# Kernel optimization log

Measured on AMD Instinct MI355X. Metric: run time of the kernel, lower is better.

The kernel has to match this reference:

```python
import jax, jax.numpy as jnp
import numpy as np

N, E, B, H, L = 50000, 500000, 64, 64, 4


def setup_inputs() -> dict:
    key = jax.random.key(0)
    ks = jax.random.split(key, 32)
    def w(k, shp, fan_in):
        s = 1.0 / np.sqrt(fan_in)
        return jax.random.uniform(k, shp, jnp.float32, -s, s)
    inp = {
        "v0": jax.random.normal(ks[0], (N, 1), jnp.float32),
        "v1": jax.random.normal(ks[1], (N, 1), jnp.float32),
        "dist": jax.random.uniform(ks[2], (E, 1), jnp.float32),
        "edge_index": jax.random.randint(ks[3], (2, E), 0, N, jnp.int32),
        "batch": jnp.sort(jax.random.randint(ks[4], (N,), 0, B, jnp.int32)),
        "batch_size": B,
        # embeddings / per-input linears
        "wte": jax.random.normal(ks[5], (2, H), jnp.float32),
        "W_in0": w(ks[6], (H, 1), 1), "b_in0": w(ks[7], (H,), 1),
        "W_in1": w(ks[8], (H, 1), 1), "b_in1": w(ks[9], (H,), 1),
        "W_out0": w(ks[10], (1, H), H), "b_out0": w(ks[11], (1,), H),
        "W_out1": w(ks[12], (1, H), H), "b_out1": w(ks[13], (1,), H),
        "W_edge": w(ks[14], (H, 1), 1), "b_edge": w(ks[15], (H,), 1),
        # shared GraphBlock (ModuleList([block]*L) shares weights)
        "W_el": w(ks[16], (H, 2 * H), 2 * H), "b_el": w(ks[17], (H,), 2 * H),
        "W_n1": w(ks[18], (4 * H, 3 * H), 3 * H), "b_n1": w(ks[19], (4 * H,), 3 * H),
        "W_n2": w(ks[20], (H, 4 * H), 4 * H), "b_n2": w(ks[21], (H,), 4 * H),
        "W_gl": w(ks[22], (H, 2 * H), 2 * H), "b_gl": w(ks[23], (H,), 2 * H),
        # shared LSTMCell
        "W_ih": w(ks[24], (4 * H, H), H), "W_hh": w(ks[25], (4 * H, H), H),
        "b_ih": w(ks[26], (4 * H,), H), "b_hh": w(ks[27], (4 * H,), H),
    }
    return inp


def _forward(v0, v1, dist, edge_index, batch, batch_size,
             wte, W_in0, b_in0, W_in1, b_in1, W_out0, b_out0, W_out1, b_out1,
             W_edge, b_edge, W_el, b_el, W_n1, b_n1, W_n2, b_n2, W_gl, b_gl,
             W_ih, W_hh, b_ih, b_hh):
    # x = sum_i (type_embedding_i + Linear_i(v_i))  -> [N, H]
    x = (wte[0] + v0 @ W_in0.T + b_in0) + (wte[1] + v1 @ W_in1.T + b_in1)
    e = dist @ W_edge.T + b_edge                      # [E, H]
    u = jnp.zeros((batch_size, x.shape[-1]), x.dtype)  # [B, H]
    row, col = edge_index[0], edge_index[1]
    n_nodes = x.shape[0]
    cs = []
    for _ in range(L):  # shared weights across layers (faithful to [block]*L)
        # edge MLP on gathered source features, scatter-max to destination nodes
        msg = jax.nn.relu(jnp.concatenate([x[row], e], axis=-1) @ W_el.T + b_el)
        agg = jax.ops.segment_max(msg, col, num_segments=n_nodes)
        agg = jnp.where(jnp.isfinite(agg), agg, 0.0)  # empty segments -> 0
        # node MLP with residual
        h1 = jax.nn.relu(jnp.concatenate([agg, x, u[batch]], axis=-1) @ W_n1.T + b_n1)
        x = x + h1 @ W_n2.T + b_n2
        # global update: per-graph max over nodes
        x_u = jax.ops.segment_max(x, batch, num_segments=batch_size)
        x_u = jnp.where(jnp.isfinite(x_u), x_u, 0.0)
        u = u + jax.nn.relu(jnp.concatenate([x_u, u], axis=-1) @ W_gl.T + b_gl)
        # LSTMCell with zero initial (h, c) every layer (hidden_states=None path)
        gates = u @ W_ih.T + b_ih + b_hh  # h_prev = 0 so W_hh term vanishes
        i_g, f_g, g_g, o_g = jnp.split(gates, 4, axis=-1)
        c = jax.nn.sigmoid(i_g) * jnp.tanh(g_g)        # c_prev = 0
        u = jax.nn.sigmoid(o_g) * jnp.tanh(c)
        cs.append(c)
    outs = jnp.stack([x @ W_out0.T + b_out0, x @ W_out1.T + b_out1])  # [2, N, 1]
    return outs, jnp.stack(cs)  # ([2,N,1], [L,B,H])


def reference(v0, v1, dist, edge_index, batch, batch_size,
              wte, W_in0, b_in0, W_in1, b_in1, W_out0, b_out0, W_out1, b_out1,
              W_edge, b_edge, W_el, b_el, W_n1, b_n1, W_n2, b_n2, W_gl, b_gl,
              W_ih, W_hh, b_ih, b_hh):
    return _forward(v0, v1, dist, edge_index, batch, batch_size,
                    wte, W_in0, b_in0, W_in1, b_in1, W_out0, b_out0, W_out1, b_out1,
                    W_edge, b_edge, W_el, b_el, W_n1, b_n1, W_n2, b_n2, W_gl, b_gl,
                    W_ih, W_hh, b_ih, b_hh)
```

## Files before the change

kernel.cpp:

```cpp
#include <hip/hip_runtime.h>


typedef __attribute__((ext_vector_type(8))) short short8;
typedef __attribute__((ext_vector_type(4))) float f32x4;

__device__ __forceinline__ unsigned short f2bf(float f) {
  union { float f; unsigned u; } v; v.f = f;
  unsigned r = v.u + 0x7FFFu + ((v.u >> 16) & 1u);
  return (unsigned short)(r >> 16);
}
__device__ __forceinline__ float bf2f(unsigned short s) {
  return __uint_as_float((unsigned)s << 16);
}
__device__ __forceinline__ unsigned enc_ordered(float f) {
  unsigned u = __float_as_uint(f);
  return (u >> 31) ? ~u : (u | 0x80000000u);
}

__global__ void k_prep_pq(const float* __restrict__ W_el, const float* __restrict__ b_el,
                          const float* __restrict__ W_edge, const float* __restrict__ b_edge,
                          const float* __restrict__ wte,
                          const float* __restrict__ Wi0, const float* __restrict__ bi0,
                          const float* __restrict__ Wi1, const float* __restrict__ bi1,
                          float* __restrict__ p, float* __restrict__ q,
                          float* __restrict__ c0, float* __restrict__ c1,
                          float* __restrict__ c2) {
  int h = threadIdx.x;
  float pp = 0.f, qq = 0.f, s0 = 0.f, s1 = 0.f, s2 = 0.f;
  for (int k = 0; k < 64; ++k) {
    float w2 = W_el[h * 128 + 64 + k];
    pp += w2 * W_edge[k];
    qq += w2 * b_edge[k];
    float w1 = W_el[h * 128 + k];
    float base = wte[k] + wte[64 + k] + bi0[k] + bi1[k];
    s0 += w1 * base;
    s1 += w1 * Wi0[k];
    s2 += w1 * Wi1[k];
  }
  p[h] = pp; q[h] = qq + b_el[h];
  c0[h] = s0; c1[h] = s1; c2[h] = s2;
}

__global__ void k_init(const float* __restrict__ v0, const float* __restrict__ v1,
                       const float* __restrict__ wte,
                       const float* __restrict__ Wi0, const float* __restrict__ bi0,
                       const float* __restrict__ Wi1, const float* __restrict__ bi1,
                       const int* __restrict__ batch,
                       int* __restrict__ gstart, int* __restrict__ gend,
                       float* __restrict__ x,
                       float* __restrict__ u, unsigned* __restrict__ xu_enc,
                       unsigned short* __restrict__ W1b, unsigned short* __restrict__ W2b,
                       unsigned short* __restrict__ Welb,
                       const float* __restrict__ W_n1, const float* __restrict__ W_n2,
                       const float* __restrict__ W_el,
                       int* __restrict__ deg, int* __restrict__ cur, int N) {
  int gt = blockIdx.x * 256 + threadIdx.x;
  int NH = N * 64;
  if (gt < NH) {
    int n = gt >> 6, h = gt & 63;
    x[gt] = wte[h] + wte[64 + h] + bi0[h] + bi1[h] + v0[n] * Wi0[h] + v1[n] * Wi1[h];
    if (h == 0) {
      int bg = batch[n];
      if (n == 0 || batch[n - 1] != bg) gstart[bg] = n;
      if (n == N - 1 || batch[n + 1] != bg) gend[bg] = n + 1;
    }
    return;
  }
  int i = gt - NH;
  if (i < 4096) {
    u[i] = 0.f;
  } else if (i < 8192) {
    xu_enc[i - 4096] = 0x007FFFFFu;
  } else if (i < 8192 + 49152) {
    int j = i - 8192;
    W1b[j] = f2bf(W_n1[j]);
  } else if (i < 8192 + 49152 + 16384) {
    int j = i - 57344;
    W2b[j] = f2bf(W_n2[j]);
  } else if (i < 77824) {
    int j = i - 73728;
    Welb[j] = f2bf(W_el[(j >> 6) * 128 + (j & 63)]);
  } else if (i < 77824 + N) {
    deg[i - 77824] = 0;
  } else if (i < 77824 + 2 * N) {
    cur[i - 77824 - N] = 0;
  }
}

__global__ __launch_bounds__(256) void k_hist(const int* __restrict__ eidx,
                                              int* __restrict__ deg, int E) {
  int e = blockIdx.x * 256 + threadIdx.x;
  if (e < E) atomicAdd(&deg[eidx[E + e]], 1);
}

__global__ __launch_bounds__(256) void k_scan1(const int* __restrict__ deg,
                                               int* __restrict__ off,
                                               int* __restrict__ bsum, int N) {
  __shared__ int s[256];
  int b = blockIdx.x, t = threadIdx.x;
  int i0 = b * 512 + t * 2;
  int v0 = (i0 < N) ? deg[i0] : 0;
  int v1 = (i0 + 1 < N) ? deg[i0 + 1] : 0;
  int sum = v0 + v1;
  s[t] = sum;
  __syncthreads();
  for (int d = 1; d < 256; d <<= 1) {
    int val = (t >= d) ? s[t - d] : 0;
    __syncthreads();
    s[t] += val;
    __syncthreads();
  }
  int excl = s[t] - sum;
  if (i0 < N) off[i0] = excl + v0;
  if (i0 + 1 < N) off[i0 + 1] = excl + v0 + v1;
  if (t == 255) bsum[b] = s[t];
}

__global__ void k_scan2(int* __restrict__ bsum, int nb) {
  __shared__ int s[128];
  int t = threadIdx.x;
  int v = (t < nb) ? bsum[t] : 0;
  s[t] = v;
  __syncthreads();
  for (int d = 1; d < 128; d <<= 1) {
    int val = (t >= d) ? s[t - d] : 0;
    __syncthreads();
    s[t] += val;
    __syncthreads();
  }
  if (t < nb) bsum[t] = s[t] - v;
}

__global__ __launch_bounds__(256) void k_scatter(const int* __restrict__ eidx,
                                                 const float* __restrict__ dist,
                                                 const int* __restrict__ off,
                                                 const int* __restrict__ bsum,
                                                 int* __restrict__ cur,
                                                 uint2* __restrict__ spack, int E) {
  int e = blockIdx.x * 256 + threadIdx.x;
  if (e >= E) return;
  int c = eidx[E + e];
  int base = (c == 0) ? 0 : (off[c - 1] + bsum[(c - 1) >> 9]);
  int pos = base + atomicAdd(&cur[c], 1);
  spack[pos] = make_uint2((unsigned)eidx[e] | ((unsigned)(c & 31) << 27),
                          __float_as_uint(dist[e]));
}

#define PROC(cc, gg)                                                     \
  do {                                                                   \
    int _c = (int)(cc);                                                  \
    if (_c != ccur) {                                                    \
      if (ccur >= 0) atomicMax(&aggi[ccur * 64 + lane], __float_as_int(m)); \
      ccur = _c; m = (gg);                                               \
    } else m = fmaxf(m, (gg));                                           \
  } while (0)

template <int MODE>
__global__ __launch_bounds__(256) void k_node(
    const int* __restrict__ off, const int* __restrict__ bsum,
    const uint2* __restrict__ spack,
    const float* __restrict__ p, const float* __restrict__ q,
    const float* __restrict__ c0, const float* __restrict__ c1,
    const float* __restrict__ c2,
    const float* __restrict__ v0, const float* __restrict__ v1,
    float* __restrict__ x, unsigned short* __restrict__ y_bf,
    const int* __restrict__ batch, const float* __restrict__ u,
    const unsigned short* __restrict__ W1b, const unsigned short* __restrict__ W2b,
    const unsigned short* __restrict__ Welb,
    const float* __restrict__ b_n1, const float* __restrict__ b_n2,
    unsigned* __restrict__ xu_enc,
    float* __restrict__ bmaxA, float* __restrict__ bmaxB,
    int* __restrict__ bgidA, int* __restrict__ bgidB,
    const float* __restrict__ Wo0, const float* __restrict__ bo0,
    const float* __restrict__ Wo1, const float* __restrict__ bo1,
    float* __restrict__ outp, int N) {
  __shared__ __align__(16) char inb[32 * 384];
  __shared__ __align__(16) char h1T[32 * 512];
  __shared__ uint2 smeta[2][128];
  __shared__ int sgb[32];
  int t = threadIdx.x;
  int n0 = blockIdx.x * 32;
  int lane = t & 63, wv = t >> 6;
  int lr = lane & 15;
  int lk8 = (lane >> 4) << 3;
  int jo = (lane >> 4) << 2;
  int swzr = (lr & 7) << 4;
  int h0 = wv * 16 + jo;

  float4 xo[2];
#pragma unroll
  for (int nt = 0; nt < 2; ++nt) {
    int node = n0 + nt * 16 + lr;
    xo[nt] = (node < N) ? *(const float4*)(x + (size_t)node * 64 + h0)
                        : make_float4(0.f, 0.f, 0.f, 0.f);
  }
  int nd_s = t >> 3, ko = t & 7;
  int node_s = n0 + nd_s;
  float4 ua = make_float4(0.f, 0.f, 0.f, 0.f), ub = ua;
  if (node_s < N) {
    int g = batch[node_s];
    const float4* u4 = (const float4*)u;
    ua = u4[g * 16 + ko * 2];
    ub = u4[g * 16 + ko * 2 + 1];
  }
  if (t < 32) sgb[t] = batch[min(n0 + t, N - 1)];
  float pv = p[lane], qv = q[lane];
  float c0v = 0.f, c1v = 0.f, c2v = 0.f;
  if (MODE == 0) { c0v = c0[lane]; c1v = c1[lane]; c2v = c2[lane]; }

  int* aggi = (int*)h1T;
#pragma unroll
  for (int i = 0; i < 8; ++i) aggi[t + i * 256] = 0;

#pragma unroll
  for (int nt = 0; nt < 2; ++nt) {
    int nd = nt * 16 + lr;
    unsigned lo = (unsigned)f2bf(xo[nt].x) | ((unsigned)f2bf(xo[nt].y) << 16);
    unsigned hi = (unsigned)f2bf(xo[nt].z) | ((unsigned)f2bf(xo[nt].w) << 16);
    *(uint2*)(inb + nd * 384 + ((128 + h0 * 2) ^ ((nd & 7) << 4))) = make_uint2(lo, hi);
  }
  {
    int swz = (nd_s & 7) << 4;
    uint4 uv;
    uv.x = f2bf(ua.x) | ((unsigned)f2bf(ua.y) << 16);
    uv.y = f2bf(ua.z) | ((unsigned)f2bf(ua.w) << 16);
    uv.z = f2bf(ub.x) | ((unsigned)f2bf(ub.y) << 16);
    uv.w = f2bf(ub.z) | ((unsigned)f2bf(ub.w) << 16);
    *(uint4*)(inb + nd_s * 384 + ((256 + ko * 16) ^ swz)) = uv;
  }

  {
    int last = min(n0 + 31, N - 1);
    int ebase = (n0 == 0) ? 0 : (off[n0 - 1] + bsum[(n0 - 1) >> 9]);
    int eend = off[last] + bsum[last >> 9];
    int total = eend - ebase;
    int nch = (total + 127) >> 7;
    if (t < 128 && t < total) smeta[0][t] = spack[ebase + t];
    float m = 0.f;
    int ccur = -1;
    __syncthreads();
    for (int c = 0; c < nch; ++c) {
      int cb = c << 7;
      int cnt = min(128, total - cb);
      if (c + 1 < nch) {
        int rem = total - cb - 128;
        if (t < 128 && t < rem) smeta[(c + 1) & 1][t] = spack[ebase + cb + 128 + t];
      }
      const uint2* sm = smeta[c & 1];
      int i = wv * 32;
      int i1 = min(i + 32, cnt);
      for (; i + 8 <= i1; i += 8) {
        uint2 e0 = sm[i], e1 = sm[i + 1], e2 = sm[i + 2], e3 = sm[i + 3];
        uint2 e4 = sm[i + 4], e5 = sm[i + 5], e6 = sm[i + 6], e7 = sm[i + 7];
        float y0, y1, y2, y3, y4, y5, y6, y7;
        if (MODE == 0) {
          int r0 = e0.x & 0x07FFFFFFu, r1 = e1.x & 0x07FFFFFFu;
          int r2 = e2.x & 0x07FFFFFFu, r3 = e3.x & 0x07FFFFFFu;
          int r4 = e4.x & 0x07FFFFFFu, r5 = e5.x & 0x07FFFFFFu;
          int r6 = e6.x & 0x07FFFFFFu, r7 = e7.x & 0x07FFFFFFu;
          y0 = fmaf(v1[r0], c2v, fmaf(v0[r0], c1v, c0v));
          y1 = fmaf(v1[r1], c2v, fmaf(v0[r1], c1v, c0v));
          y2 = fmaf(v1[r2], c2v, fmaf(v0[r2], c1v, c0v));
          y3 = fmaf(v1[r3], c2v, fmaf(v0[r3], c1v, c0v));
          y4 = fmaf(v1[r4], c2v, fmaf(v0[r4], c1v, c0v));
          y5 = fmaf(v1[r5], c2v, fmaf(v0[r5], c1v, c0v));
          y6 = fmaf(v1[r6], c2v, fmaf(v0[r6], c1v, c0v));
          y7 = fmaf(v1[r7], c2v, fmaf(v0[r7], c1v, c0v));
        } else {
          y0 = bf2f(y_bf[(int)((e0.x & 0x07FFFFFFu) << 6) + lane]);
          y1 = bf2f(y_bf[(int)((e1.x & 0x07FFFFFFu) << 6) + lane]);
          y2 = bf2f(y_bf[(int)((e2.x & 0x07FFFFFFu) << 6) + lane]);
          y3 = bf2f(y_bf[(int)((e3.x & 0x07FFFFFFu) << 6) + lane]);
          y4 = bf2f(y_bf[(int)((e4.x & 0x07FFFFFFu) << 6) + lane]);
          y5 = bf2f(y_bf[(int)((e5.x & 0x07FFFFFFu) << 6) + lane]);
          y6 = bf2f(y_bf[(int)((e6.x & 0x07FFFFFFu) << 6) + lane]);
          y7 = bf2f(y_bf[(int)((e7.x & 0x07FFFFFFu) << 6) + lane]);
        }
        float g0 = fmaxf(fmaf(__uint_as_float(e0.y), pv, y0 + qv), 0.f);
        float g1 = fmaxf(fmaf(__uint_as_float(e1.y), pv, y1 + qv), 0.f);
        float g2 = fmaxf(fmaf(__uint_as_float(e2.y), pv, y2 + qv), 0.f);
        float g3 = fmaxf(fmaf(__uint_as_float(e3.y), pv, y3 + qv), 0.f);
        float g4 = fmaxf(fmaf(__uint_as_float(e4.y), pv, y4 + qv), 0.f);
        float g5 = fmaxf(fmaf(__uint_as_float(e5.y), pv, y5 + qv), 0.f);
        float g6 = fmaxf(fmaf(__uint_as_float(e6.y), pv, y6 + qv), 0.f);
        float g7 = fmaxf(fmaf(__uint_as_float(e7.y), pv, y7 + qv), 0.f);
        PROC(e0.x >> 27, g0); PROC(e1.x >> 27, g1);
        PROC(e2.x >> 27, g2); PROC(e3.x >> 27, g3);
        PROC(e4.x >> 27, g4); PROC(e5.x >> 27, g5);
        PROC(e6.x >> 27, g6); PROC(e7.x >> 27, g7);
      }
      for (; i < i1; ++i) {
        uint2 e0 = sm[i];
        float y0;
        if (MODE == 0) {
          int r0 = e0.x & 0x07FFFFFFu;
          y0 = fmaf(v1[r0], c2v, fmaf(v0[r0], c1v, c0v));
        } else {
          y0 = bf2f(y_bf[(int)((e0.x & 0x07FFFFFFu) << 6) + lane]);
        }
        float g0 = fmaxf(fmaf(__uint_as_float(e0.y), pv, y0 + qv), 0.f);
        PROC(e0.x >> 27, g0);
      }
      __syncthreads();
    }
    if (ccur >= 0) atomicMax(&aggi[ccur * 64 + lane], __float_as_int(m));
  }
  __syncthreads();

  {
    int swz = (nd_s & 7) << 4;
    const float4* ag4 = (const float4*)(h1T);
    float4 aa = ag4[nd_s * 16 + ko * 2];
    float4 ab = ag4[nd_s * 16 + ko * 2 + 1];
    uint4 av;
    av.x = f2bf(aa.x) | ((unsigned)f2bf(aa.y) << 16);
    av.y = f2bf(aa.z) | ((unsigned)f2bf(aa.w) << 16);
    av.z = f2bf(ab.x) | ((unsigned)f2bf(ab.y) << 16);
    av.w = f2bf(ab.z) | ((unsigned)f2bf(ab.w) << 16);
    *(uint4*)(inb + nd_s * 384 + ((ko * 16) ^ swz)) = av;
  }
  __syncthreads();

  int w = wv;

  f32x4 acc[4][2];
#pragma unroll
  for (int ot = 0; ot < 4; ++ot)
#pragma unroll
    for (int nt = 0; nt < 2; ++nt) acc[ot][nt] = (f32x4){0.f, 0.f, 0.f, 0.f};
  const unsigned short* W1p = W1b + (w * 64 + lr) * 192 + lk8;
#pragma unroll
  for (int ks = 0; ks < 6; ++ks) {
    int kb = ks * 64 + lk8 * 2;
    short8 b0 = *(const short8*)(inb + lr * 384 + (kb ^ swzr));
    short8 b1 = *(const short8*)(inb + (16 + lr) * 384 + (kb ^ swzr));
#pragma unroll
    for (int ot = 0; ot < 4; ++ot) {
      short8 a = *(const short8*)(W1p + ot * (16 * 192) + ks * 32);
      acc[ot][0] = __builtin_amdgcn_mfma_f32_16x16x32_bf16(a, b0, acc[ot][0], 0, 0, 0);
      acc[ot][1] = __builtin_amdgcn_mfma_f32_16x16x32_bf16(a, b1, acc[ot][1], 0, 0, 0);
    }
  }
  __syncthreads();
#pragma unroll
  for (int ot = 0; ot < 4; ++ot) {
    int o = w * 64 + ot * 16 + jo;
    float4 bs = *(const float4*)(b_n1 + o);
#pragma unroll
    for (int nt = 0; nt < 2; ++nt) {
      int nd = nt * 16 + lr;
      unsigned lo = (unsigned)f2bf(fmaxf(acc[ot][nt][0] + bs.x, 0.f)) |
                    ((unsigned)f2bf(fmaxf(acc[ot][nt][1] + bs.y, 0.f)) << 16);
      unsigned hi = (unsigned)f2bf(fmaxf(acc[ot][nt][2] + bs.z, 0.f)) |
                    ((unsigned)f2bf(fmaxf(acc[ot][nt][3] + bs.w, 0.f)) << 16);
      *(uint2*)(h1T + nd * 512 + ((o * 2) ^ ((nd & 7) << 4))) = make_uint2(lo, hi);
    }
  }
  __syncthreads();

  f32x4 acc2[2] = {{0.f, 0.f, 0.f, 0.f}, {0.f, 0.f, 0.f, 0.f}};
  const unsigned short* W2p = W2b + (w * 16 + lr) * 256 + lk8;
#pragma unroll
  for (int ks = 0; ks < 8; ++ks) {
    short8 a = *(const short8*)(W2p + ks * 32);
    int kb = ks * 64 + lk8 * 2;
    short8 b0 = *(const short8*)(h1T + lr * 512 + (kb ^ swzr));
    short8 b1 = *(const short8*)(h1T + (16 + lr) * 512 + (kb ^ swzr));
    acc2[0] = __builtin_amdgcn_mfma_f32_16x16x32_bf16(a, b0, acc2[0], 0, 0, 0);
    acc2[1] = __builtin_amdgcn_mfma_f32_16x16x32_bf16(a, b1, acc2[1], 0, 0, 0);
  }
  float4 b2 = *(const float4*)(b_n2 + h0);
  char* xnb = inb;
  float4 xn[2];
#pragma unroll
  for (int nt = 0; nt < 2; ++nt) {
    int nd = nt * 16 + lr;
    int node = n0 + nd;
    xn[nt].x = xo[nt].x + acc2[nt][0] + b2.x;
    xn[nt].y = xo[nt].y + acc2[nt][1] + b2.y;
    xn[nt].z = xo[nt].z + acc2[nt][2] + b2.z;
    xn[nt].w = xo[nt].w + acc2[nt][3] + b2.w;
    if (node >= N) xn[nt] = make_float4(0.f, 0.f, 0.f, 0.f);
    if (MODE != 2 && node < N) *(float4*)(x + (size_t)node * 64 + h0) = xn[nt];
    if (MODE != 2) {
      unsigned lo = (unsigned)f2bf(xn[nt].x) | ((unsigned)f2bf(xn[nt].y) << 16);
      unsigned hi = (unsigned)f2bf(xn[nt].z) | ((unsigned)f2bf(xn[nt].w) << 16);
      *(uint2*)(xnb + nd * 128 + ((h0 * 2) ^ ((nd & 7) << 4))) = make_uint2(lo, hi);
    }
  }

  {
    const float NEG = -__builtin_huge_valf();
    int gA = sgb[0], gB = sgb[31];
    float a0 = NEG, a1 = NEG, a2 = NEG, a3 = NEG;
    float e0 = NEG, e1 = NEG, e2 = NEG, e3 = NEG;
#pragma unroll
    for (int nt = 0; nt < 2; ++nt) {
      int nd = nt * 16 + lr;
      if (n0 + nd < N) {
        int g = sgb[nd];
        if (g == gA) {
          a0 = fmaxf(a0, xn[nt].x); a1 = fmaxf(a1, xn[nt].y);
          a2 = fmaxf(a2, xn[nt].z); a3 = fmaxf(a3, xn[nt].w);
        } else if (g == gB) {
          e0 = fmaxf(e0, xn[nt].x); e1 = fmaxf(e1, xn[nt].y);
          e2 = fmaxf(e2, xn[nt].z); e3 = fmaxf(e3, xn[nt].w);
        } else {
          unsigned* xe = xu_enc + g * 64 + h0;
          atomicMax(xe + 0, enc_ordered(xn[nt].x));
          atomicMax(xe + 1, enc_ordered(xn[nt].y));
          atomicMax(xe + 2, enc_ordered(xn[nt].z));
          atomicMax(xe + 3, enc_ordered(xn[nt].w));
        }
      }
    }
#pragma unroll
    for (int msk = 1; msk <= 8; msk <<= 1) {
      a0 = fmaxf(a0, __shfl_xor(a0, msk)); a1 = fmaxf(a1, __shfl_xor(a1, msk));
      a2 = fmaxf(a2, __shfl_xor(a2, msk)); a3 = fmaxf(a3, __shfl_xor(a3, msk));
      e0 = fmaxf(e0, __shfl_xor(e0, msk)); e1 = fmaxf(e1, __shfl_xor(e1, msk));
      e2 = fmaxf(e2, __shfl_xor(e2, msk)); e3 = fmaxf(e3, __shfl_xor(e3, msk));
    }
    if (lr == 0) {
      size_t base = (size_t)blockIdx.x * 64 + h0;
      bmaxA[base + 0] = a0; bmaxA[base + 1] = a1;
      bmaxA[base + 2] = a2; bmaxA[base + 3] = a3;
      bmaxB[base + 0] = e0; bmaxB[base + 1] = e1;
      bmaxB[base + 2] = e2; bmaxB[base + 3] = e3;
    }
    if (t == 0) {
      bgidA[blockIdx.x] = gA;
      bgidB[blockIdx.x] = (gB == gA) ? -1 : gB;
    }
  }
  __syncthreads();

  if (MODE != 2) {
    f32x4 acc3[2] = {{0.f, 0.f, 0.f, 0.f}, {0.f, 0.f, 0.f, 0.f}};
    const unsigned short* W3p = Welb + (w * 16 + lr) * 64 + lk8;
#pragma unroll
    for (int ks = 0; ks < 2; ++ks) {
      short8 a = *(const short8*)(W3p + ks * 32);
      int kb = ks * 64 + lk8 * 2;
      short8 b0 = *(const short8*)(xnb + lr * 128 + (kb ^ swzr));
      short8 b1 = *(const short8*)(xnb + (16 + lr) * 128 + (kb ^ swzr));
      acc3[0] = __builtin_amdgcn_mfma_f32_16x16x32_bf16(a, b0, acc3[0], 0, 0, 0);
      acc3[1] = __builtin_amdgcn_mfma_f32_16x16x32_bf16(a, b1, acc3[1], 0, 0, 0);
    }
    int o0 = w * 16 + jo;
#pragma unroll
    for (int nt = 0; nt < 2; ++nt) {
      int node = n0 + nt * 16 + lr;
      if (node < N) {
        unsigned lo = (unsigned)f2bf(acc3[nt][0]) | ((unsigned)f2bf(acc3[nt][1]) << 16);
        unsigned hi = (unsigned)f2bf(acc3[nt][2]) | ((unsigned)f2bf(acc3[nt][3]) << 16);
        *(uint2*)(y_bf + (size_t)node * 64 + o0) = make_uint2(lo, hi);
      }
    }
  } else {
    float4 w0 = *(const float4*)(Wo0 + h0);
    float4 w1 = *(const float4*)(Wo1 + h0);
    float* ow = (float*)h1T;
#pragma unroll
    for (int nt = 0; nt < 2; ++nt) {
      float p0 = xn[nt].x * w0.x + xn[nt].y * w0.y + xn[nt].z * w0.z + xn[nt].w * w0.w;
      float p1 = xn[nt].x * w1.x + xn[nt].y * w1.y + xn[nt].z * w1.z + xn[nt].w * w1.w;
      p0 += __shfl_xor(p0, 16); p0 += __shfl_xor(p0, 32);
      p1 += __shfl_xor(p1, 16); p1 += __shfl_xor(p1, 32);
      if (lane < 16) {
        ow[w * 64 + 0 + nt * 16 + lr] = p0;
        ow[w * 64 + 32 + nt * 16 + lr] = p1;
      }
    }
    __syncthreads();
    if (t < 64) {
      int oi = t >> 5, nd = t & 31;
      int node = n0 + nd;
      if (node < N) {
        float v = ow[0 * 64 + oi * 32 + nd] + ow[1 * 64 + oi * 32 + nd] +
                  ow[2 * 64 + oi * 32 + nd] + ow[3 * 64 + oi * 32 + nd];
        v += (oi ? bo1[0] : bo0[0]);
        outp[(size_t)oi * N + node] = v;
      }
    }
  }
}

__global__ __launch_bounds__(64) void k_graph(const int* __restrict__ gstart,
                                              const int* __restrict__ gend,
                                              const float* __restrict__ bmaxA,
                                              const float* __restrict__ bmaxB,
                                              const int* __restrict__ bgidA,
                                              const int* __restrict__ bgidB,
                                              unsigned* __restrict__ xu_enc,
                                              float* __restrict__ u,
                                              const float* __restrict__ W_gl,
                                              const float* __restrict__ b_gl,
                                              const float* __restrict__ W_ih,
                                              const float* __restrict__ b_ih,
                                              const float* __restrict__ b_hh,
                                              float* __restrict__ c_out) {
  __shared__ float xu_s[64], us[64], un[64];
  int g = blockIdx.x, h = threadIdx.x;
  float m = -__builtin_huge_valf();
  int gs = gstart[g], ge = gend[g];
  if (gs < ge) {
    int bs = gs >> 5, be = (ge - 1) >> 5;
    for (int b = bs; b <= be; ++b) {
      if (bgidA[b] == g) m = fmaxf(m, bmaxA[(size_t)b * 64 + h]);
      if (bgidB[b] == g) m = fmaxf(m, bmaxB[(size_t)b * 64 + h]);
    }
  }
  {
    unsigned Ev = xu_enc[g * 64 + h];
    float fd = (Ev & 0x80000000u) ? __uint_as_float(Ev & 0x7FFFFFFFu)
                                  : __uint_as_float(~Ev);
    m = fmaxf(m, fd);
    xu_enc[g * 64 + h] = 0x007FFFFFu;
  }
  float f = isfinite(m) ? m : 0.f;
  xu_s[h] = f;
  float uo = u[g * 64 + h];
  us[h] = uo;
  __syncthreads();
  float pre = b_gl[h];
  for (int k = 0; k < 64; ++k) pre += xu_s[k] * W_gl[h * 128 + k];
  for (int k = 0; k < 64; ++k) pre += us[k] * W_gl[h * 128 + 64 + k];
  float unew = uo + fmaxf(pre, 0.f);
  un[h] = unew;
  __syncthreads();
  float gi = b_ih[h] + b_hh[h];
  float gg = b_ih[128 + h] + b_hh[128 + h];
  float go = b_ih[192 + h] + b_hh[192 + h];
  for (int k = 0; k < 64; ++k) {
    float uv = un[k];
    gi += uv * W_ih[h * 64 + k];
    gg += uv * W_ih[(128 + h) * 64 + k];
    go += uv * W_ih[(192 + h) * 64 + k];
  }
  float cc = (1.f / (1.f + expf(-gi))) * tanhf(gg);
  float u2v = (1.f / (1.f + expf(-go))) * tanhf(cc);
  c_out[g * 64 + h] = cc;
  u[g * 64 + h] = u2v;
}

extern "C" void kernel_launch(void* const* d_in, const int* in_sizes, int n_in,
                              void* d_out, int out_size, void* d_ws, size_t ws_size,
                              hipStream_t stream) {
  const float* v0 = (const float*)d_in[0];
  const float* v1 = (const float*)d_in[1];
  const float* dist = (const float*)d_in[2];
  const int* eidx = (const int*)d_in[3];
  const int* batch = (const int*)d_in[4];
  const float* wte = (const float*)d_in[6];
  const float* Wi0 = (const float*)d_in[7];
  const float* bi0 = (const float*)d_in[8];
  const float* Wi1 = (const float*)d_in[9];
  const float* bi1 = (const float*)d_in[10];
  const float* Wo0 = (const float*)d_in[11];
  const float* bo0 = (const float*)d_in[12];
  const float* Wo1 = (const float*)d_in[13];
  const float* bo1 = (const float*)d_in[14];
  const float* W_edge = (const float*)d_in[15];
  const float* b_edge = (const float*)d_in[16];
  const float* W_el = (const float*)d_in[17];
  const float* b_el = (const float*)d_in[18];
  const float* W_n1 = (const float*)d_in[19];
  const float* b_n1 = (const float*)d_in[20];
  const float* W_n2 = (const float*)d_in[21];
  const float* b_n2 = (const float*)d_in[22];
  const float* W_gl = (const float*)d_in[23];
  const float* b_gl = (const float*)d_in[24];
  const float* W_ih = (const float*)d_in[25];
  const float* b_ih = (const float*)d_in[27];
  const float* b_hh = (const float*)d_in[28];

  const int N = in_sizes[0];
  const int E = in_sizes[2];
  const int NH = N * 64;
  const int NB512 = (N + 511) / 512;
  const int nblk = (N + 31) / 32;

  float* ws = (float*)d_ws;
  float* x = ws;
  float* u = x + NH;
  unsigned* xu_enc = (unsigned*)(u + 4096);
  float* p = (float*)(xu_enc + 4096);
  float* q = p + 64;
  float* c0 = q + 64;
  float* c1 = c0 + 64;
  float* c2 = c1 + 64;
  unsigned short* W1b = (unsigned short*)(c2 + 64);
  unsigned short* W2b = W1b + 49152;
  unsigned short* Welb = W2b + 16384;
  unsigned short* y_bf = Welb + 4096;
  int* deg = (int*)(y_bf + NH);
  int* off = deg + N;
  int* cur = off + N;
  int* bsum = cur + N;
  int* gstart = bsum + 128;
  int* gend = gstart + 64;
  int* bgidA = gend + 64;
  int* bgidB = bgidA + nblk;
  float* bmaxA = (float*)(bgidB + nblk);
  float* bmaxB = bmaxA + (size_t)nblk * 64;
  uint2* spack = (uint2*)(((size_t)(bmaxB + (size_t)nblk * 64) + 15) & ~(size_t)15);

  float* outp = (float*)d_out;

  k_prep_pq<<<1, 64, 0, stream>>>(W_el, b_el, W_edge, b_edge, wte, Wi0, bi0, Wi1, bi1,
                                  p, q, c0, c1, c2);
  k_init<<<(NH + 77824 + 2 * N + 255) / 256, 256, 0, stream>>>(
      v0, v1, wte, Wi0, bi0, Wi1, bi1, batch, gstart, gend, x,
      u, xu_enc, W1b, W2b, Welb, W_n1, W_n2, W_el, deg, cur, N);
  k_hist<<<(E + 255) / 256, 256, 0, stream>>>(eidx, deg, E);
  k_scan1<<<NB512, 256, 0, stream>>>(deg, off, bsum, N);
  k_scan2<<<1, 128, 0, stream>>>(bsum, NB512);
  k_scatter<<<(E + 255) / 256, 256, 0, stream>>>(eidx, dist, off, bsum, cur, spack, E);

  for (int l = 0; l < 4; ++l) {
    if (l == 0) {
      k_node<0><<<nblk, 256, 0, stream>>>(off, bsum, spack, p, q, c0, c1, c2, v0, v1,
                                          x, y_bf, batch, u, W1b, W2b, Welb, b_n1, b_n2,
                                          xu_enc, bmaxA, bmaxB, bgidA, bgidB,
                                          Wo0, bo0, Wo1, bo1, outp, N);
    } else if (l < 3) {
      k_node<1><<<nblk, 256, 0, stream>>>(off, bsum, spack, p, q, c0, c1, c2, v0, v1,
                                          x, y_bf, batch, u, W1b, W2b, Welb, b_n1, b_n2,
                                          xu_enc, bmaxA, bmaxB, bgidA, bgidB,
                                          Wo0, bo0, Wo1, bo1, outp, N);
    } else {
      k_node<2><<<nblk, 256, 0, stream>>>(off, bsum, spack, p, q, c0, c1, c2, v0, v1,
                                          x, y_bf, batch, u, W1b, W2b, Welb, b_n1, b_n2,
                                          xu_enc, bmaxA, bmaxB, bgidA, bgidB,
                                          Wo0, bo0, Wo1, bo1, outp, N);
    }
    k_graph<<<64, 64, 0, stream>>>(gstart, gend, bmaxA, bmaxB, bgidA, bgidB,
                                   xu_enc, u, W_gl, b_gl, W_ih, b_ih, b_hh,
                                   outp + 2 * N + l * 4096);
  }
}
```

Baseline: 370.5 us.

## Give each wave its own edge range in gather and widen graph kernel

New measurement: 337.5 us. -8.9%, faster.

```diff
diff --git a/kernel.cpp b/kernel.cpp
--- a/kernel.cpp
+++ b/kernel.cpp
@@ -176,7 +176,7 @@
     float* __restrict__ outp, int N) {
   __shared__ __align__(16) char inb[32 * 384];
   __shared__ __align__(16) char h1T[32 * 512];
-  __shared__ uint2 smeta[2][128];
+  __shared__ uint2 smeta[256];
   __shared__ int sgb[32];
   int t = threadIdx.x;
   int n0 = blockIdx.x * 32;
@@ -228,28 +228,35 @@
     uv.w = f2bf(ub.z) | ((unsigned)f2bf(ub.w) << 16);
     *(uint4*)(inb + nd_s * 384 + ((256 + ko * 16) ^ swz)) = uv;
   }
+  __syncthreads();
 
   {
     int last = min(n0 + 31, N - 1);
     int ebase = (n0 == 0) ? 0 : (off[n0 - 1] + bsum[(n0 - 1) >> 9]);
     int eend = off[last] + bsum[last >> 9];
     int total = eend - ebase;
-    int nch = (total + 127) >> 7;
-    if (t < 128 && t < total) smeta[0][t] = spack[ebase + t];
+    int q4 = total >> 2;
+    int wb = ebase + wv * q4;
+    int we = (wv == 3) ? eend : (wb + q4);
+    uint2* sm = smeta + wv * 64;
+    const unsigned short* ybl = y_bf + lane;
     float m = 0.f;
     int ccur = -1;
-    __syncthreads();
-    for (int c = 0; c < nch; ++c) {
-      int cb = c << 7;
-      int cnt = min(128, total - cb);
-      if (c + 1 < nch) {
-        int rem = total - cb - 128;
-        if (t < 128 && t < rem) smeta[(c + 1) & 1][t] = spack[ebase + cb + 128 + t];
+    uint2 r = make_uint2(0u, 0u);
+    if (wb < we) {
+      int cnt = min(64, we - wb);
+      if (lane < cnt) r = spack[wb + lane];
+    }
+    for (int cb = wb; cb < we; cb += 64) {
+      int ccnt = min(64, we - cb);
+      sm[lane] = r;
+      int nb = cb + 64;
+      if (nb < we) {
+        int ncnt = we - nb;
+        if (lane < ncnt) r = spack[nb + lane];
       }
-      const uint2* sm = smeta[c & 1];
-      int i = wv * 32;
-      int i1 = min(i + 32, cnt);
-      for (; i + 8 <= i1; i += 8) {
+      int i = 0;
+      for (; i + 8 <= ccnt; i += 8) {
         uint2 e0 = sm[i], e1 = sm[i + 1], e2 = sm[i + 2], e3 = sm[i + 3];
         uint2 e4 = sm[i + 4], e5 = sm[i + 5], e6 = sm[i + 6], e7 = sm[i + 7];
         float y0, y1, y2, y3, y4, y5, y6, y7;
@@ -267,14 +274,14 @@
           y6 = fmaf(v1[r6], c2v, fmaf(v0[r6], c1v, c0v));
           y7 = fmaf(v1[r7], c2v, fmaf(v0[r7], c1v, c0v));
         } else {
-          y0 = bf2f(y_bf[(int)((e0.x & 0x07FFFFFFu) << 6) + lane]);
-          y1 = bf2f(y_bf[(int)((e1.x & 0x07FFFFFFu) << 6) + lane]);
-          y2 = bf2f(y_bf[(int)((e2.x & 0x07FFFFFFu) << 6) + lane]);
-          y3 = bf2f(y_bf[(int)((e3.x & 0x07FFFFFFu) << 6) + lane]);
-          y4 = bf2f(y_bf[(int)((e4.x & 0x07FFFFFFu) << 6) + lane]);
-          y5 = bf2f(y_bf[(int)((e5.x & 0x07FFFFFFu) << 6) + lane]);
-          y6 = bf2f(y_bf[(int)((e6.x & 0x07FFFFFFu) << 6) + lane]);
-          y7 = bf2f(y_bf[(int)((e7.x & 0x07FFFFFFu) << 6) + lane]);
+          y0 = bf2f(ybl[(int)((e0.x & 0x07FFFFFFu) << 6)]);
+          y1 = bf2f(ybl[(int)((e1.x & 0x07FFFFFFu) << 6)]);
+          y2 = bf2f(ybl[(int)((e2.x & 0x07FFFFFFu) << 6)]);
+          y3 = bf2f(ybl[(int)((e3.x & 0x07FFFFFFu) << 6)]);
+          y4 = bf2f(ybl[(int)((e4.x & 0x07FFFFFFu) << 6)]);
+          y5 = bf2f(ybl[(int)((e5.x & 0x07FFFFFFu) << 6)]);
+          y6 = bf2f(ybl[(int)((e6.x & 0x07FFFFFFu) << 6)]);
+          y7 = bf2f(ybl[(int)((e7.x & 0x07FFFFFFu) << 6)]);
         }
         float g0 = fmaxf(fmaf(__uint_as_float(e0.y), pv, y0 + qv), 0.f);
         float g1 = fmaxf(fmaf(__uint_as_float(e1.y), pv, y1 + qv), 0.f);
@@ -289,19 +296,18 @@
         PROC(e4.x >> 27, g4); PROC(e5.x >> 27, g5);
         PROC(e6.x >> 27, g6); PROC(e7.x >> 27, g7);
       }
-      for (; i < i1; ++i) {
+      for (; i < ccnt; ++i) {
         uint2 e0 = sm[i];
         float y0;
         if (MODE == 0) {
           int r0 = e0.x & 0x07FFFFFFu;
           y0 = fmaf(v1[r0], c2v, fmaf(v0[r0], c1v, c0v));
         } else {
-          y0 = bf2f(y_bf[(int)((e0.x & 0x07FFFFFFu) << 6) + lane]);
+          y0 = bf2f(ybl[(int)((e0.x & 0x07FFFFFFu) << 6)]);
         }
         float g0 = fmaxf(fmaf(__uint_as_float(e0.y), pv, y0 + qv), 0.f);
         PROC(e0.x >> 27, g0);
       }
-      __syncthreads();
     }
     if (ccur >= 0) atomicMax(&aggi[ccur * 64 + lane], __float_as_int(m));
   }
@@ -486,62 +492,85 @@
   }
 }
 
-__global__ __launch_bounds__(64) void k_graph(const int* __restrict__ gstart,
-                                              const int* __restrict__ gend,
-                                              const float* __restrict__ bmaxA,
-                                              const float* __restrict__ bmaxB,
-                                              const int* __restrict__ bgidA,
-                                              const int* __restrict__ bgidB,
-                                              unsigned* __restrict__ xu_enc,
-                                              float* __restrict__ u,
-                                              const float* __restrict__ W_gl,
-                                              const float* __restrict__ b_gl,
-                                              const float* __restrict__ W_ih,
-                                              const float* __restrict__ b_ih,
-                                              const float* __restrict__ b_hh,
-                                              float* __restrict__ c_out) {
+__global__ __launch_bounds__(256) void k_graph(const int* __restrict__ gstart,
+                                               const int* __restrict__ gend,
+                                               const float* __restrict__ bmaxA,
+                                               const float* __restrict__ bmaxB,
+                                               const int* __restrict__ bgidA,
+                                               const int* __restrict__ bgidB,
+                                               unsigned* __restrict__ xu_enc,
+                                               float* __restrict__ u,
+                                               const float* __restrict__ W_gl,
+                                               const float* __restrict__ b_gl,
+                                               const float* __restrict__ W_ih,
+                                               const float* __restrict__ b_ih,
+                                               const float* __restrict__ b_hh,
+                                               float* __restrict__ c_out) {
+  __shared__ float red[4][3][64];
   __shared__ float xu_s[64], us[64], un[64];
-  int g = blockIdx.x, h = threadIdx.x;
-  float m = -__builtin_huge_valf();
+  int g = blockIdx.x;
+  int t = threadIdx.x, h = t & 63, qd = t >> 6;
+  const float NEG = -__builtin_huge_valf();
+
+  float m = NEG;
   int gs = gstart[g], ge = gend[g];
   if (gs < ge) {
     int bs = gs >> 5, be = (ge - 1) >> 5;
-    for (int b = bs; b <= be; ++b) {
+    for (int b = bs + qd; b <= be; b += 4) {
       if (bgidA[b] == g) m = fmaxf(m, bmaxA[(size_t)b * 64 + h]);
       if (bgidB[b] == g) m = fmaxf(m, bmaxB[(size_t)b * 64 + h]);
     }
   }
-  {
+  red[qd][0][h] = m;
+  __syncthreads();
+  if (qd == 0) {
+    m = fmaxf(fmaxf(red[0][0][h], red[1][0][h]), fmaxf(red[2][0][h], red[3][0][h]));
     unsigned Ev = xu_enc[g * 64 + h];
     float fd = (Ev & 0x80000000u) ? __uint_as_float(Ev & 0x7FFFFFFFu)
                                   : __uint_as_float(~Ev);
     m = fmaxf(m, fd);
     xu_enc[g * 64 + h] = 0x007FFFFFu;
-  }
-  float f = isfinite(m) ? m : 0.f;
-  xu_s[h] = f;
-  float uo = u[g * 64 + h];
-  us[h] = uo;
-  __syncthreads();
-  float pre = b_gl[h];
-  for (int k = 0; k < 64; ++k) pre += xu_s[k] * W_gl[h * 128 + k];
-  for (int k = 0; k < 64; ++k) pre += us[k] * W_gl[h * 128 + 64 + k];
-  float unew = uo + fmaxf(pre, 0.f);
-  un[h] = unew;
-  __syncthreads();
-  float gi = b_ih[h] + b_hh[h];
-  float gg = b_ih[128 + h] + b_hh[128 + h];
-  float go = b_ih[192 + h] + b_hh[192 + h];
-  for (int k = 0; k < 64; ++k) {
+    xu_s[h] = isfinite(m) ? m : 0.f;
+    us[h] = u[g * 64 + h];
+  }
+  __syncthreads();
+
+  float pre = 0.f;
+  {
+    const float* Wrow = W_gl + h * 128 + qd * 32;
+    const float* src = (qd < 2) ? (xu_s + qd * 32) : (us + (qd - 2) * 32);
+#pragma unroll 8
+    for (int k = 0; k < 32; ++k) pre += src[k] * Wrow[k];
+  }
+  red[qd][0][h] = pre;
+  __syncthreads();
+  if (qd == 0) {
+    float prs = red[0][0][h] + red[1][0][h] + red[2][0][h] + red[3][0][h] + b_gl[h];
+    un[h] = us[h] + fmaxf(prs, 0.f);
+  }
+  __syncthreads();
+
+  float gi = 0.f, gg = 0.f, go = 0.f;
+#pragma unroll 4
+  for (int k = qd * 16; k < qd * 16 + 16; ++k) {
     float uv = un[k];
     gi += uv * W_ih[h * 64 + k];
     gg += uv * W_ih[(128 + h) * 64 + k];
     go += uv * W_ih[(192 + h) * 64 + k];
   }
-  float cc = (1.f / (1.f + expf(-gi))) * tanhf(gg);
-  float u2v = (1.f / (1.f + expf(-go))) * tanhf(cc);
-  c_out[g * 64 + h] = cc;
-  u[g * 64 + h] = u2v;
+  red[qd][0][h] = gi; red[qd][1][h] = gg; red[qd][2][h] = go;
+  __syncthreads();
+  if (qd == 0) {
+    gi = red[0][0][h] + red[1][0][h] + red[2][0][h] + red[3][0][h] + b_ih[h] + b_hh[h];
+    gg = red[0][1][h] + red[1][1][h] + red[2][1][h] + red[3][1][h] +
+         b_ih[128 + h] + b_hh[128 + h];
+    go = red[0][2][h] + red[1][2][h] + red[2][2][h] + red[3][2][h] +
+         b_ih[192 + h] + b_hh[192 + h];
+    float cc = (1.f / (1.f + expf(-gi))) * tanhf(gg);
+    float u2v = (1.f / (1.f + expf(-go))) * tanhf(cc);
+    c_out[g * 64 + h] = cc;
+    u[g * 64 + h] = u2v;
+  }
 }
 
 extern "C" void kernel_launch(void* const* d_in, const int* in_sizes, int n_in,
@@ -635,8 +664,8 @@
                                           xu_enc, bmaxA, bmaxB, bgidA, bgidB,
                                           Wo0, bo0, Wo1, bo1, outp, N);
     }
-    k_graph<<<64, 64, 0, stream>>>(gstart, gend, bmaxA, bmaxB, bgidA, bgidB,
-                                   xu_enc, u, W_gl, b_gl, W_ih, b_ih, b_hh,
-                                   outp + 2 * N + l * 4096);
-  }
-}
+    k_graph<<<64, 256, 0, stream>>>(gstart, gend, bmaxA, bmaxB, bgidA, bgidB,
+                                    xu_enc, u, W_gl, b_gl, W_ih, b_ih, b_hh,
+                                    outp + 2 * N + l * 4096);
+  }
+}
```
